# Optimization experiments

Hardware: AMD Instinct MI355X
Metric: run time of the kernel (lower is better)

## Reference

```python
import jax, jax.numpy as jnp
import numpy as np

B, L = 128, 100
VOCAB, WORD_D = 50000, 100
TAG_NUM, TAG_D = 52, 20
POS_NUM, POS_D = 202, 20
HID = 256                 # hidden_size = NUM_CAPS * CAP_D
NUM_CAPS, CAP_D = 16, 16
N_CLASS = 19
ROUTING_ITER = 3
IN_D = WORD_D + TAG_D + 2 * POS_D  # 160
ENTITY_MARK = 68          # pos value marking the entity token


def setup_inputs() -> dict:
    key = jax.random.key(0)
    ks = jax.random.split(key, 20)
    s = 0.05
    word = jax.random.randint(ks[0], (B, L), 0, VOCAB)
    tag = jax.random.randint(ks[1], (B, L), 0, TAG_NUM)
    pos1 = jax.random.randint(ks[2], (B, L), 0, POS_NUM)
    pos2 = jax.random.randint(ks[3], (B, L), 0, POS_NUM)
    # guarantee exactly one ENTITY_MARK per row (getEntityFeature's .index(68))
    pos1 = jnp.where(pos1 == ENTITY_MARK, ENTITY_MARK + 1, pos1)
    pos2 = jnp.where(pos2 == ENTITY_MARK, ENTITY_MARK + 1, pos2)
    e1 = jax.random.randint(ks[4], (B,), 0, L)
    e2 = jax.random.randint(ks[5], (B,), 0, L)
    pos1 = pos1.at[jnp.arange(B), e1].set(ENTITY_MARK)
    pos2 = pos2.at[jnp.arange(B), e2].set(ENTITY_MARK)
    # embedding tables (padding_idx 0 rows zeroed for tag/pos, as in torch)
    word_emb = jax.random.normal(ks[6], (VOCAB, WORD_D), jnp.float32) * s
    tag_emb = (jax.random.normal(ks[7], (TAG_NUM, TAG_D), jnp.float32) * s).at[0].set(0.0)
    pos1_emb = (jax.random.normal(ks[8], (POS_NUM, POS_D), jnp.float32) * s).at[0].set(0.0)
    pos2_emb = (jax.random.normal(ks[9], (POS_NUM, POS_D), jnp.float32) * s).at[0].set(0.0)
    # BiLSTM params (torch gate order i,f,g,o stacked along first axis)
    def lstm_params(k):
        k1, k2 = jax.random.split(k)
        w_ih = jax.random.normal(k1, (4 * HID, IN_D), jnp.float32) * s
        w_hh = jax.random.normal(k2, (4 * HID, HID), jnp.float32) * s
        return w_ih, w_hh, jnp.zeros((4 * HID,), jnp.float32), jnp.zeros((4 * HID,), jnp.float32)
    w_ih_f, w_hh_f, b_ih_f, b_hh_f = lstm_params(ks[10])
    w_ih_b, w_hh_b, b_ih_b, b_hh_b = lstm_params(ks[11])
    # digit-caps transform [in_caps, in_dim, out_caps*out_dim]
    W_caps = jax.random.normal(ks[12], (NUM_CAPS * L, CAP_D, N_CLASS * CAP_D), jnp.float32) * s
    b_route = jnp.zeros((NUM_CAPS * L, N_CLASS), jnp.float32)  # routing logit prior (learned)
    return {"word": word, "tag": tag, "pos1": pos1, "pos2": pos2,
            "word_emb": word_emb, "tag_emb": tag_emb, "pos1_emb": pos1_emb, "pos2_emb": pos2_emb,
            "w_ih_f": w_ih_f, "w_hh_f": w_hh_f, "b_ih_f": b_ih_f, "b_hh_f": b_hh_f,
            "w_ih_b": w_ih_b, "w_hh_b": w_hh_b, "b_ih_b": b_ih_b, "b_hh_b": b_hh_b,
            "W_caps": W_caps, "b_route": b_route}


def _lstm_dir(x, w_ih, w_hh, b_ih, b_hh, reverse):
    # x: [B, L, IN_D] -> h: [B, L, HID]
    xg = jnp.einsum('bld,gd->blg', x, w_ih) + b_ih + b_hh  # precompute input gates
    def step(carry, g):
        h, c = carry
        g = g + h @ w_hh.T
        i, f, gg, o = jnp.split(g, 4, axis=-1)
        c = jax.nn.sigmoid(f) * c + jax.nn.sigmoid(i) * jnp.tanh(gg)
        h = jax.nn.sigmoid(o) * jnp.tanh(c)
        return (h, c), h
    init = (jnp.zeros((x.shape[0], HID), x.dtype), jnp.zeros((x.shape[0], HID), x.dtype))
    _, hs = jax.lax.scan(step, init, jnp.swapaxes(xg, 0, 1), reverse=reverse)
    return jnp.swapaxes(hs, 0, 1)


def _squash(x, axis=-1):
    n2 = jnp.sum(x * x, axis=axis, keepdims=True)
    return x * (n2 / (1.0 + n2)) / jnp.sqrt(n2 + 1e-9)


def reference(word, tag, pos1, pos2, word_emb, tag_emb, pos1_emb, pos2_emb,
              w_ih_f, w_hh_f, b_ih_f, b_hh_f, w_ih_b, w_hh_b, b_ih_b, b_hh_b,
              W_caps, b_route):
    # embed + concat (dropout = identity in eval mode)
    emb = jnp.concatenate([word_emb[word], tag_emb[tag], pos1_emb[pos1], pos2_emb[pos2]], axis=-1)
    hf = _lstm_dir(emb, w_ih_f, w_hh_f, b_ih_f, b_hh_f, reverse=False)
    hb = _lstm_dir(emb, w_ih_b, w_hh_b, b_ih_b, b_hh_b, reverse=True)
    x = hf + hb  # sum of direction halves == x[:,:,:H] + x[:,:,H:2H]
    # vectorized entity gather: first index where pos == 68
    bidx = jnp.arange(x.shape[0])
    e1 = jnp.argmax(pos1 == ENTITY_MARK, axis=1)
    e2 = jnp.argmax(pos2 == ENTITY_MARK, axis=1)
    he = x[bidx, e1] + x[bidx, e2]  # [B, HID]
    # primary capsules: [B, L*NUM_CAPS, CAP_D], squashed per capsule
    u = _squash(x.reshape(x.shape[0], L * NUM_CAPS, CAP_D))
    # entity-guided attention over words, broadcast to capsules
    att = jax.nn.softmax(jnp.einsum('bld,bd->bl', x, he), axis=1)  # [B, L]
    alpha = jnp.repeat(att, NUM_CAPS, axis=1)  # [B, L*NUM_CAPS]
    # digit caps predictions: [B, in_caps, N_CLASS, CAP_D]
    u_hat = jnp.einsum('bic,ico->bio', u, W_caps).reshape(x.shape[0], L * NUM_CAPS, N_CLASS, CAP_D)
    # attention-weighted agreement routing
    bb = jnp.broadcast_to(b_route, (x.shape[0],) + b_route.shape)
    v = None
    for _ in range(ROUTING_ITER):
        c = jax.nn.softmax(bb, axis=-1) * alpha[:, :, None]  # coupling * attention
        s = jnp.einsum('bio,biod->bod', c, u_hat)
        v = _squash(s)  # [B, N_CLASS, CAP_D]
        bb = bb + jnp.einsum('biod,bod->bio', u_hat, v)
    # class probabilities = capsule lengths
    return jnp.sqrt(jnp.sum(v * v, axis=2) + 1e-9)
```

## Files before the change

### kernel.cpp

```cpp
#include <hip/hip_runtime.h>
#include <math.h>

#define B_     128
#define L_     100
#define HID_   256
#define IND_   160
#define NCLASS 19
#define CAPD   16
#define NI     1600
#define OD     304
#define ENTITY 68

#define SLDS   24

typedef _Float16 half2_t __attribute__((ext_vector_type(2)));

__device__ inline half2_t as_h2(unsigned u) {
    union { unsigned u; half2_t h; } x; x.u = u; return x.h;
}
__device__ inline unsigned pack2(float a, float b) {
    union { unsigned u; half2_t h; } x;
    x.h = (half2_t){ (_Float16)a, (_Float16)b };
    return x.u;
}
__device__ inline float fdot2_(unsigned w, unsigned h, float acc) {
#if __has_builtin(__builtin_amdgcn_fdot2)
    return __builtin_amdgcn_fdot2(as_h2(w), as_h2(h), acc, false);
#else
    half2_t wh = as_h2(w), hh = as_h2(h);
    acc = fmaf((float)wh.x, (float)hh.x, acc);
    return fmaf((float)wh.y, (float)hh.y, acc);
#endif
}

__global__ void emb_gather(const int* __restrict__ word, const int* __restrict__ tag,
                           const int* __restrict__ pos1, const int* __restrict__ pos2,
                           const float* __restrict__ we, const float* __restrict__ te,
                           const float* __restrict__ p1e, const float* __restrict__ p2e,
                           float* __restrict__ emb)
{
    int idx = blockIdx.x * 256 + threadIdx.x;
    int bt = idx / IND_;
    int k  = idx - bt * IND_;
    float v;
    if (k < 100)      v = we[word[bt] * 100 + k];
    else if (k < 120) v = te[tag[bt] * 20 + (k - 100)];
    else if (k < 140) v = p1e[pos1[bt] * 20 + (k - 120)];
    else              v = p2e[pos2[bt] * 20 + (k - 140)];
    emb[idx] = v;
}

__global__ void __launch_bounds__(256) gemm_xg(
    const float* __restrict__ emb,
    const float* __restrict__ wihf, const float* __restrict__ bihf, const float* __restrict__ bhhf,
    const float* __restrict__ wihb, const float* __restrict__ bihb, const float* __restrict__ bhhb,
    float* __restrict__ xg)
{
    int gt  = blockIdx.x;
    int t   = blockIdx.y;
    int dir = blockIdx.z;
    const float* w  = dir ? wihb : wihf;
    const float* bi = dir ? bihb : bihf;
    const float* bh = dir ? bhhb : bhhf;
    int gj0 = gt * 128;

    __shared__ float wsh[32][132];
    __shared__ float esh[32][132];

    int tid = threadIdx.x;
    int tx = tid & 15, ty = tid >> 4;

    float acc[8][8];
    #pragma unroll
    for (int i = 0; i < 8; ++i)
        #pragma unroll
        for (int j = 0; j < 8; ++j) acc[i][j] = 0.f;

    for (int k0 = 0; k0 < IND_; k0 += 32) {
        __syncthreads();
        #pragma unroll
        for (int m = 0; m < 16; ++m) {
            int e = m * 256 + tid;
            int k = e & 31, g = e >> 5;
            wsh[k][g] = w[(gj0 + g) * IND_ + k0 + k];
            esh[k][g] = emb[(g * L_ + t) * IND_ + k0 + k];
        }
        __syncthreads();
        #pragma unroll
        for (int k = 0; k < 32; ++k) {
            float wv[8], ev[8];
            #pragma unroll
            for (int q = 0; q < 8; ++q) wv[q] = wsh[k][ty * 8 + q];
            #pragma unroll
            for (int q = 0; q < 8; ++q) ev[q] = esh[k][tx * 8 + q];
            #pragma unroll
            for (int i = 0; i < 8; ++i)
                #pragma unroll
                for (int j = 0; j < 8; ++j) acc[i][j] = fmaf(wv[i], ev[j], acc[i][j]);
        }
    }
    #pragma unroll
    for (int i = 0; i < 8; ++i) {
        int gj = gj0 + ty * 8 + i;
        float bias = bi[gj] + bh[gj];
        #pragma unroll
        for (int j = 0; j < 8; ++j) {
            int b = tx * 8 + j;
            xg[((((size_t)dir * L_ + t) * 64 + (b >> 1)) * 1024 + gj) * 2 + (b & 1)]
                = acc[i][j] + bias;
        }
    }
}

__global__ void whh_pack16(const float* __restrict__ whhf, const float* __restrict__ whhb,
                           unsigned* __restrict__ wp)
{
    int gid = blockIdx.x * 256 + threadIdx.x;
    int g   = gid & 3;
    int h   = (gid >> 2) & 255;
    int p   = (gid >> 10) & 127;
    int dir = gid >> 17;
    const float* whh = dir ? whhb : whhf;
    const float* row = whh + (size_t)(g * 256 + h) * HID_;
    wp[gid] = pack2(row[2 * p], row[2 * p + 1]);
}

__global__ void __launch_bounds__(1024, 4) lstm_scan_s(
    const float* __restrict__ xg, const uint4* __restrict__ wp16,
    float* __restrict__ xf2, float* __restrict__ xb2)
{
    int blk = blockIdx.x;
    int dir = blk >> 6;
    int bp  = blk & 63;
    int tid = threadIdx.x;
    int h   = tid & 255;
    int q   = tid >> 8;

    const uint4* wt = wp16 + (size_t)dir * 128 * 256;
    float* xo = dir ? xb2 : xf2;

    __shared__ uint2 hA[128];
    __shared__ uint2 hB[128];
    __shared__ float pbuf[4][8][256];
    __shared__ uint4 wlds[SLDS][256];

    for (int m = q; m < SLDS; m += 4)
        wlds[m][h] = wt[m * 256 + h];

    if (tid < 256) ((unsigned*)hA)[tid] = 0u;
    float c0 = 0.f, c1 = 0.f;
    __syncthreads();

    int pq0  = q * 32;
    int sbeg = (q == 0) ? SLDS : pq0;
    int send = pq0 + 32;

    for (int t = 0; t < L_; ++t) {
        int slot = dir ? (L_ - 1 - t) : t;
        const uint2* hp = (t & 1) ? hB : hA;
        unsigned*    hw = (unsigned*)((t & 1) ? hA : hB);

        float2 gI, gF, gG, gO;
        if (q == 0) {
            const float* xbase = xg + (((size_t)dir * L_ + slot) * 64 + bp) * 2048;
            gI = *(const float2*)(xbase + (0 * 256 + h) * 2);
            gF = *(const float2*)(xbase + (1 * 256 + h) * 2);
            gG = *(const float2*)(xbase + (2 * 256 + h) * 2);
            gO = *(const float2*)(xbase + (3 * 256 + h) * 2);
        }

        float aI0=0.f, aI1=0.f, aF0=0.f, aF1=0.f;
        float aG0=0.f, aG1=0.f, aO0=0.f, aO1=0.f;

        #pragma unroll 8
        for (int p = sbeg; p < send; ++p) {
            uint4 w4 = wt[p * 256 + h];
            uint2 hb = hp[p];
            aI0 = fdot2_(w4.x, hb.x, aI0); aI1 = fdot2_(w4.x, hb.y, aI1);
            aF0 = fdot2_(w4.y, hb.x, aF0); aF1 = fdot2_(w4.y, hb.y, aF1);
            aG0 = fdot2_(w4.z, hb.x, aG0); aG1 = fdot2_(w4.z, hb.y, aG1);
            aO0 = fdot2_(w4.w, hb.x, aO0); aO1 = fdot2_(w4.w, hb.y, aO1);
        }
        if (q == 0) {
            #pragma unroll 8
            for (int p = 0; p < SLDS; ++p) {
                uint4 w4 = wlds[p][h];
                uint2 hb = hp[p];
                aI0 = fdot2_(w4.x, hb.x, aI0); aI1 = fdot2_(w4.x, hb.y, aI1);
                aF0 = fdot2_(w4.y, hb.x, aF0); aF1 = fdot2_(w4.y, hb.y, aF1);
                aG0 = fdot2_(w4.z, hb.x, aG0); aG1 = fdot2_(w4.z, hb.y, aG1);
                aO0 = fdot2_(w4.w, hb.x, aO0); aO1 = fdot2_(w4.w, hb.y, aO1);
            }
        }

        pbuf[q][0][h] = aI0; pbuf[q][1][h] = aI1;
        pbuf[q][2][h] = aF0; pbuf[q][3][h] = aF1;
        pbuf[q][4][h] = aG0; pbuf[q][5][h] = aG1;
        pbuf[q][6][h] = aO0; pbuf[q][7][h] = aO1;
        __syncthreads();

        if (q == 0) {
            float sI0 = pbuf[0][0][h] + pbuf[1][0][h] + pbuf[2][0][h] + pbuf[3][0][h] + gI.x;
            float sI1 = pbuf[0][1][h] + pbuf[1][1][h] + pbuf[2][1][h] + pbuf[3][1][h] + gI.y;
            float sF0 = pbuf[0][2][h] + pbuf[1][2][h] + pbuf[2][2][h] + pbuf[3][2][h] + gF.x;
            float sF1 = pbuf[0][3][h] + pbuf[1][3][h] + pbuf[2][3][h] + pbuf[3][3][h] + gF.y;
            float sG0 = pbuf[0][4][h] + pbuf[1][4][h] + pbuf[2][4][h] + pbuf[3][4][h] + gG.x;
            float sG1 = pbuf[0][5][h] + pbuf[1][5][h] + pbuf[2][5][h] + pbuf[3][5][h] + gG.y;
            float sO0 = pbuf[0][6][h] + pbuf[1][6][h] + pbuf[2][6][h] + pbuf[3][6][h] + gO.x;
            float sO1 = pbuf[0][7][h] + pbuf[1][7][h] + pbuf[2][7][h] + pbuf[3][7][h] + gO.y;

            float i0 = 1.f / (1.f + expf(-sI0));
            float f0 = 1.f / (1.f + expf(-sF0));
            float g0 = tanhf(sG0);
            float o0 = 1.f / (1.f + expf(-sO0));
            c0 = f0 * c0 + i0 * g0;
            float hv0 = o0 * tanhf(c0);

            float i1 = 1.f / (1.f + expf(-sI1));
            float f1 = 1.f / (1.f + expf(-sF1));
            float g1 = tanhf(sG1);
            float o1 = 1.f / (1.f + expf(-sO1));
            c1 = f1 * c1 + i1 * g1;
            float hv1 = o1 * tanhf(c1);

            float n0 = __shfl_xor(hv0, 1);
            float n1 = __shfl_xor(hv1, 1);
            hw[h] = (h & 1) ? pack2(n1, hv1)
                            : pack2(hv0, n0);
            float* xp = xo + ((size_t)slot * 64 + bp) * 512 + h * 2;
            xp[0] = hv0; xp[1] = hv1;
        }
        __syncthreads();
    }
}

__global__ void x_add(const float* __restrict__ xf2, const float* __restrict__ xb2,
                      float* __restrict__ x)
{
    int idx = blockIdx.x * 256 + threadIdx.x;
    int b    = idx & 127;
    int j    = (idx >> 7) & 255;
    int slot = idx >> 15;
    int src  = ((slot * 64 + (b >> 1)) * 512) + j * 2 + (b & 1);
    x[idx] = xf2[src] + xb2[src];
}

__global__ void wc_pack16(const float* __restrict__ W, unsigned* __restrict__ wc)
{
    int gid = blockIdx.x * 256 + threadIdx.x;
    int od  = gid % OD;
    int rest = gid / OD;
    int cp  = rest & 7;
    int i   = rest >> 3;
    float a = W[((size_t)i * 16 + 2 * cp) * OD + od];
    float b = W[((size_t)i * 16 + 2 * cp + 1) * OD + od];
    wc[gid] = pack2(a, b);
}

__global__ void find_entity(const int* __restrict__ pos1, const int* __restrict__ pos2,
                            int* __restrict__ e)
{
    int b = threadIdx.x;
    int e1 = 0, e2 = 0;
    for (int l = L_ - 1; l >= 0; --l) if (pos1[b * L_ + l] == ENTITY) e1 = l;
    for (int l = L_ - 1; l >= 0; --l) if (pos2[b * L_ + l] == ENTITY) e2 = l;
    e[b] = e1; e[B_ + b] = e2;
}

__global__ void compute_he(const float* __restrict__ x, const int* __restrict__ e,
                           float* __restrict__ he)
{
    int j = blockIdx.x, b = threadIdx.x;
    int e1 = e[b], e2 = e[B_ + b];
    he[j * B_ + b] = x[((size_t)e1 * HID_ + j) * B_ + b] + x[((size_t)e2 * HID_ + j) * B_ + b];
}

__global__ void att_logits(const float* __restrict__ x, const float* __restrict__ he,
                           float* __restrict__ logits)
{
    int l = blockIdx.x, b = threadIdx.x;
    float acc = 0.f;
    for (int j = 0; j < HID_; ++j)
        acc = fmaf(x[((size_t)l * HID_ + j) * B_ + b], he[j * B_ + b], acc);
    logits[l * B_ + b] = acc;
}

__global__ void att_softmax(const float* __restrict__ logits, float* __restrict__ att)
{
    int b = threadIdx.x;
    float m = -1e30f;
    for (int l = 0; l < L_; ++l) m = fmaxf(m, logits[l * B_ + b]);
    float s = 0.f;
    for (int l = 0; l < L_; ++l) s += expf(logits[l * B_ + b] - m);
    float inv = 1.f / s;
    for (int l = 0; l < L_; ++l) att[l * B_ + b] = expf(logits[l * B_ + b] - m) * inv;
}

__global__ void u_squash16(const float* __restrict__ x, unsigned* __restrict__ u16)
{
    int i = blockIdx.x, b = threadIdx.x;
    int l = i >> 4, cap = i & 15;
    float vals[16]; float n2 = 0.f;
    #pragma unroll
    for (int c2 = 0; c2 < 16; ++c2) {
        float v = x[((size_t)l * HID_ + cap * 16 + c2) * B_ + b];
        vals[c2] = v; n2 = fmaf(v, v, n2);
    }
    float f = (n2 / (1.f + n2)) / sqrtf(n2 + 1e-9f);
    #pragma unroll
    for (int cp = 0; cp < 8; ++cp)
        u16[((size_t)i * B_ + b) * 8 + cp] = pack2(vals[2 * cp] * f, vals[2 * cp + 1] * f);
}

__global__ void bb_init(const float* __restrict__ br, float* __restrict__ bb)
{
    int idx = blockIdx.x * 256 + threadIdx.x;
    bb[idx] = br[idx % (NI * NCLASS)];
}

__global__ void __launch_bounds__(320) s_pass16(
    const unsigned* __restrict__ u16, const unsigned* __restrict__ Wc16,
    const float* __restrict__ bb, const float* __restrict__ att,
    float* __restrict__ partial)
{
    int ic = blockIdx.x, bt = blockIdx.y;
    int i0 = ic * 16, b0 = bt * 16;
    __shared__ float C[16][16][20];
    int tid = threadIdx.x;
    if (tid < 256) {
        int bl = tid >> 4, il = tid & 15;
        int b = b0 + bl, i = i0 + il;
        const float* bbp = bb + ((size_t)b * NI + i) * NCLASS;
        float m = bbp[0];
        #pragma unroll
        for (int o = 1; o < NCLASS; ++o) m = fmaxf(m, bbp[o]);
        float s = 0.f; float e[NCLASS];
        #pragma unroll
        for (int o = 0; o < NCLASS; ++o) { e[o] = expf(bbp[o] - m); s += e[o]; }
        float al = att[(i >> 4) * B_ + b] / s;
        #pragma unroll
        for (int o = 0; o < NCLASS; ++o) C[bl][il][o] = e[o] * al;
    }
    __syncthreads();
    if (tid >= OD) return;
    int od = tid, o = od >> 4;
    float acc[16];
    #pragma unroll
    for (int bl = 0; bl < 16; ++bl) acc[bl] = 0.f;
    for (int il = 0; il < 16; ++il) {
        int i = i0 + il;
        const unsigned* wp = Wc16 + (size_t)i * 8 * OD + od;
        unsigned w2[8];
        #pragma unroll
        for (int cp = 0; cp < 8; ++cp) w2[cp] = wp[cp * OD];
        const unsigned* up = u16 + ((size_t)i * B_ + b0) * 8;
        #pragma unroll
        for (int bl = 0; bl < 16; ++bl) {
            float uh = 0.f;
            #pragma unroll
            for (int cp = 0; cp < 8; ++cp) uh = fdot2_(up[bl * 8 + cp], w2[cp], uh);
            acc[bl] = fmaf(C[bl][il][o], uh, acc[bl]);
        }
    }
    #pragma unroll
    for (int bl = 0; bl < 16; ++bl)
        partial[((size_t)ic * B_ + b0 + bl) * OD + od] = acc[bl];
}

__global__ void s_reduce(const float* __restrict__ partial, float* __restrict__ s)
{
    int idx = blockIdx.x * 256 + threadIdx.x;
    int b = idx / OD, od = idx - b * OD;
    float acc = 0.f;
    for (int ic = 0; ic < 100; ++ic) acc += partial[((size_t)ic * B_ + b) * OD + od];
    s[idx] = acc;
}

__global__ void squash_v(const float* __restrict__ s, float* __restrict__ v,
                         float* __restrict__ out, int write_out)
{
    int idx = blockIdx.x * 256 + threadIdx.x;
    if (idx >= B_ * NCLASS) return;
    const float* sp = s + (size_t)idx * 16;
    float vals[16]; float n2 = 0.f;
    #pragma unroll
    for (int d = 0; d < 16; ++d) { vals[d] = sp[d]; n2 = fmaf(vals[d], vals[d], n2); }
    float f = (n2 / (1.f + n2)) / sqrtf(n2 + 1e-9f);
    float n2v = 0.f;
    #pragma unroll
    for (int d = 0; d < 16; ++d) {
        float vv = vals[d] * f;
        v[(size_t)idx * 16 + d] = vv;
        n2v = fmaf(vv, vv, n2v);
    }
    if (write_out) out[idx] = sqrtf(n2v + 1e-9f);
}

__global__ void __launch_bounds__(320) bb_pass16(
    const unsigned* __restrict__ u16, const unsigned* __restrict__ Wc16,
    const float* __restrict__ v, float* __restrict__ bb)
{
    int ic = blockIdx.x, bt = blockIdx.y;
    int i0 = ic * 16, b0 = bt * 16;
    int tid = threadIdx.x;
    if (tid >= OD) return;
    int od = tid, o = od >> 4, d = od & 15;
    float vv[16];
    #pragma unroll
    for (int bl = 0; bl < 16; ++bl) vv[bl] = v[(size_t)(b0 + bl) * OD + od];
    for (int il = 0; il < 16; ++il) {
        int i = i0 + il;
        const unsigned* wp = Wc16 + (size_t)i * 8 * OD + od;
        unsigned w2[8];
        #pragma unroll
        for (int cp = 0; cp < 8; ++cp) w2[cp] = wp[cp * OD];
        const unsigned* up = u16 + ((size_t)i * B_ + b0) * 8;
        #pragma unroll
        for (int bl = 0; bl < 16; ++bl) {
            float uh = 0.f;
            #pragma unroll
            for (int cp = 0; cp < 8; ++cp) uh = fdot2_(up[bl * 8 + cp], w2[cp], uh);
            float p = uh * vv[bl];
            p += __shfl_xor(p, 1);
            p += __shfl_xor(p, 2);
            p += __shfl_xor(p, 4);
            p += __shfl_xor(p, 8);
            if (d == 0) bb[((size_t)(b0 + bl) * NI + i) * NCLASS + o] += p;
        }
    }
}

extern "C" void kernel_launch(void* const* d_in, const int* in_sizes, int n_in,
                              void* d_out, int out_size, void* d_ws, size_t ws_size,
                              hipStream_t stream)
{
    (void)in_sizes; (void)n_in; (void)out_size; (void)ws_size;
    const int*   word = (const int*)d_in[0];
    const int*   tag  = (const int*)d_in[1];
    const int*   pos1 = (const int*)d_in[2];
    const int*   pos2 = (const int*)d_in[3];
    const float* we   = (const float*)d_in[4];
    const float* te   = (const float*)d_in[5];
    const float* p1e  = (const float*)d_in[6];
    const float* p2e  = (const float*)d_in[7];
    const float* wihf = (const float*)d_in[8];
    const float* whhf = (const float*)d_in[9];
    const float* bihf = (const float*)d_in[10];
    const float* bhhf = (const float*)d_in[11];
    const float* wihb = (const float*)d_in[12];
    const float* whhb = (const float*)d_in[13];
    const float* bihb = (const float*)d_in[14];
    const float* bhhb = (const float*)d_in[15];
    const float* Wc   = (const float*)d_in[16];
    const float* br   = (const float*)d_in[17];

    float* wsp    = (float*)d_ws;
    float* emb    = wsp;
    float* xg     = wsp + 2048000;
    float* xf     = xg + 26214400;
    float* xb     = xf + 3276800;
    float* he     = xb + 3276800;
    float* logits = he + 32768;
    float* att    = logits + 12800;
    int*   e      = (int*)(att + 12800);
    unsigned* wp16 = (unsigned*)emb;
    unsigned* Wc16 = (unsigned*)xf;
    float*    x    = xg;
    unsigned* u16  = (unsigned*)(xg + 3276800);
    float*    bb   = xg + 6553600;
    float*    part = xg + 10444800;
    float*    s    = xg + 14336000;
    float*    v    = s + 38912;
    float*    out  = (float*)d_out;

    emb_gather<<<8000, 256, 0, stream>>>(word, tag, pos1, pos2, we, te, p1e, p2e, emb);
    gemm_xg<<<dim3(8, 100, 2), 256, 0, stream>>>(emb, wihf, bihf, bhhf, wihb, bihb, bhhb, xg);
    whh_pack16<<<1024, 256, 0, stream>>>(whhf, whhb, wp16);
    lstm_scan_s<<<128, 1024, 0, stream>>>(xg, (const uint4*)wp16, xf, xb);
    x_add<<<12800, 256, 0, stream>>>(xf, xb, x);
    wc_pack16<<<15200, 256, 0, stream>>>(Wc, Wc16);
    find_entity<<<1, 128, 0, stream>>>(pos1, pos2, e);
    compute_he<<<256, 128, 0, stream>>>(x, e, he);
    att_logits<<<100, 128, 0, stream>>>(x, he, logits);
    att_softmax<<<1, 128, 0, stream>>>(logits, att);
    u_squash16<<<1600, 128, 0, stream>>>(x, u16);
    bb_init<<<15200, 256, 0, stream>>>(br, bb);
    for (int it = 0; it < 3; ++it) {
        s_pass16<<<dim3(100, 8), 320, 0, stream>>>(u16, Wc16, bb, att, part);
        s_reduce<<<152, 256, 0, stream>>>(part, s);
        squash_v<<<10, 256, 0, stream>>>(s, v, out, (it == 2) ? 1 : 0);
        if (it < 2) bb_pass16<<<dim3(100, 8), 320, 0, stream>>>(u16, Wc16, v, bb);
    }
}
```

Measured before the change: 1.174 ms.

## Use fp16 dot2 input GEMM, fold bb init, parallelize attention softmax

```diff
diff --git a/kernel.cpp b/kernel.cpp
--- a/kernel.cpp
+++ b/kernel.cpp
@@ -33,39 +33,53 @@
 #endif
 }
 
-__global__ void emb_gather(const int* __restrict__ word, const int* __restrict__ tag,
-                           const int* __restrict__ pos1, const int* __restrict__ pos2,
-                           const float* __restrict__ we, const float* __restrict__ te,
-                           const float* __restrict__ p1e, const float* __restrict__ p2e,
-                           float* __restrict__ emb)
+__global__ void emb_gather16(const int* __restrict__ word, const int* __restrict__ tag,
+                             const int* __restrict__ pos1, const int* __restrict__ pos2,
+                             const float* __restrict__ we, const float* __restrict__ te,
+                             const float* __restrict__ p1e, const float* __restrict__ p2e,
+                             unsigned* __restrict__ emb16)
 {
     int idx = blockIdx.x * 256 + threadIdx.x;
-    int bt = idx / IND_;
-    int k  = idx - bt * IND_;
-    float v;
-    if (k < 100)      v = we[word[bt] * 100 + k];
-    else if (k < 120) v = te[tag[bt] * 20 + (k - 100)];
-    else if (k < 140) v = p1e[pos1[bt] * 20 + (k - 120)];
-    else              v = p2e[pos2[bt] * 20 + (k - 140)];
-    emb[idx] = v;
-}
-
-__global__ void __launch_bounds__(256) gemm_xg(
-    const float* __restrict__ emb,
-    const float* __restrict__ wihf, const float* __restrict__ bihf, const float* __restrict__ bhhf,
-    const float* __restrict__ wihb, const float* __restrict__ bihb, const float* __restrict__ bhhb,
+    int bt = idx / 80;
+    int kp = idx - bt * 80;
+    int k  = 2 * kp;
+    float v0, v1;
+    if (k < 100)      { const float* p = we  + word[bt] * 100 + k;         v0 = p[0]; v1 = p[1]; }
+    else if (k < 120) { const float* p = te  + tag[bt]  * 20 + (k - 100);  v0 = p[0]; v1 = p[1]; }
+    else if (k < 140) { const float* p = p1e + pos1[bt] * 20 + (k - 120);  v0 = p[0]; v1 = p[1]; }
+    else              { const float* p = p2e + pos2[bt] * 20 + (k - 140);  v0 = p[0]; v1 = p[1]; }
+    emb16[idx] = pack2(v0, v1);
+}
+
+__global__ void wih_pack16(const float* __restrict__ wihf, const float* __restrict__ wihb,
+                           unsigned* __restrict__ wp)
+{
+    int gid = blockIdx.x * 256 + threadIdx.x;
+    int dir = gid / 81920;
+    int rem = gid - dir * 81920;
+    int kp  = rem >> 10;
+    int gj  = rem & 1023;
+    const float* w = dir ? wihb : wihf;
+    const float* row = w + (size_t)gj * IND_ + 2 * kp;
+    wp[gid] = pack2(row[0], row[1]);
+}
+
+__global__ void __launch_bounds__(256) gemm_xg16(
+    const unsigned* __restrict__ emb16, const unsigned* __restrict__ wih16,
+    const float* __restrict__ bihf, const float* __restrict__ bhhf,
+    const float* __restrict__ bihb, const float* __restrict__ bhhb,
     float* __restrict__ xg)
 {
     int gt  = blockIdx.x;
     int t   = blockIdx.y;
     int dir = blockIdx.z;
-    const float* w  = dir ? wihb : wihf;
+    const unsigned* wbase = wih16 + (size_t)dir * 81920;
     const float* bi = dir ? bihb : bihf;
     const float* bh = dir ? bhhb : bhhf;
     int gj0 = gt * 128;
 
-    __shared__ float wsh[32][132];
-    __shared__ float esh[32][132];
+    __shared__ unsigned wsh[16][132];
+    __shared__ unsigned esh[16][132];
 
     int tid = threadIdx.x;
     int tx = tid & 15, ty = tid >> 4;
@@ -76,27 +90,28 @@
         #pragma unroll
         for (int j = 0; j < 8; ++j) acc[i][j] = 0.f;
 
-    for (int k0 = 0; k0 < IND_; k0 += 32) {
+    for (int kp0 = 0; kp0 < 80; kp0 += 16) {
         __syncthreads();
         #pragma unroll
-        for (int m = 0; m < 16; ++m) {
+        for (int m = 0; m < 8; ++m) {
             int e = m * 256 + tid;
-            int k = e & 31, g = e >> 5;
-            wsh[k][g] = w[(gj0 + g) * IND_ + k0 + k];
-            esh[k][g] = emb[(g * L_ + t) * IND_ + k0 + k];
+            int kw = e >> 7, gw = e & 127;
+            wsh[kw][gw] = wbase[(kp0 + kw) * 1024 + gj0 + gw];
+            int ke = e & 15, ge = e >> 4;
+            esh[ke][ge] = emb16[((size_t)ge * L_ + t) * 80 + kp0 + ke];
         }
         __syncthreads();
         #pragma unroll
-        for (int k = 0; k < 32; ++k) {
-            float wv[8], ev[8];
+        for (int kp = 0; kp < 16; ++kp) {
+            unsigned wv[8], ev[8];
             #pragma unroll
-            for (int q = 0; q < 8; ++q) wv[q] = wsh[k][ty * 8 + q];
+            for (int q = 0; q < 8; ++q) wv[q] = wsh[kp][ty * 8 + q];
             #pragma unroll
-            for (int q = 0; q < 8; ++q) ev[q] = esh[k][tx * 8 + q];
+            for (int q = 0; q < 8; ++q) ev[q] = esh[kp][tx * 8 + q];
             #pragma unroll
             for (int i = 0; i < 8; ++i)
                 #pragma unroll
-                for (int j = 0; j < 8; ++j) acc[i][j] = fmaf(wv[i], ev[j], acc[i][j]);
+                for (int j = 0; j < 8; ++j) acc[i][j] = fdot2_(wv[i], ev[j], acc[i][j]);
         }
     }
     #pragma unroll
@@ -257,43 +272,56 @@
     wc[gid] = pack2(a, b);
 }
 
-__global__ void find_entity(const int* __restrict__ pos1, const int* __restrict__ pos2,
-                            int* __restrict__ e)
-{
-    int b = threadIdx.x;
+__global__ void compute_he2(const int* __restrict__ pos1, const int* __restrict__ pos2,
+                            const float* __restrict__ x, float* __restrict__ he)
+{
+    int j = blockIdx.x, b = threadIdx.x;
     int e1 = 0, e2 = 0;
     for (int l = L_ - 1; l >= 0; --l) if (pos1[b * L_ + l] == ENTITY) e1 = l;
     for (int l = L_ - 1; l >= 0; --l) if (pos2[b * L_ + l] == ENTITY) e2 = l;
-    e[b] = e1; e[B_ + b] = e2;
-}
-
-__global__ void compute_he(const float* __restrict__ x, const int* __restrict__ e,
-                           float* __restrict__ he)
-{
-    int j = blockIdx.x, b = threadIdx.x;
-    int e1 = e[b], e2 = e[B_ + b];
     he[j * B_ + b] = x[((size_t)e1 * HID_ + j) * B_ + b] + x[((size_t)e2 * HID_ + j) * B_ + b];
 }
 
-__global__ void att_logits(const float* __restrict__ x, const float* __restrict__ he,
-                           float* __restrict__ logits)
-{
-    int l = blockIdx.x, b = threadIdx.x;
+__global__ void att_logits2(const float* __restrict__ x, const float* __restrict__ he,
+                            float* __restrict__ lp)
+{
+    int l = blockIdx.x, jc = blockIdx.y, b = threadIdx.x;
+    int j0 = jc * 32;
     float acc = 0.f;
-    for (int j = 0; j < HID_; ++j)
+    #pragma unroll
+    for (int jj = 0; jj < 32; ++jj) {
+        int j = j0 + jj;
         acc = fmaf(x[((size_t)l * HID_ + j) * B_ + b], he[j * B_ + b], acc);
-    logits[l * B_ + b] = acc;
-}
-
-__global__ void att_softmax(const float* __restrict__ logits, float* __restrict__ att)
-{
-    int b = threadIdx.x;
-    float m = -1e30f;
-    for (int l = 0; l < L_; ++l) m = fmaxf(m, logits[l * B_ + b]);
-    float s = 0.f;
-    for (int l = 0; l < L_; ++l) s += expf(logits[l * B_ + b] - m);
-    float inv = 1.f / s;
-    for (int l = 0; l < L_; ++l) att[l * B_ + b] = expf(logits[l * B_ + b] - m) * inv;
+    }
+    lp[((size_t)jc * L_ + l) * B_ + b] = acc;
+}
+
+__global__ void att_softmax2(const float* __restrict__ lp, float* __restrict__ att)
+{
+    int b = blockIdx.x, l = threadIdx.x;
+    float val = 0.f;
+    if (l < L_) {
+        #pragma unroll
+        for (int jc = 0; jc < 8; ++jc) val += lp[((size_t)jc * L_ + l) * B_ + b];
+    }
+    __shared__ float red[128];
+    red[l] = (l < L_) ? val : -1e30f;
+    __syncthreads();
+    for (int off = 64; off > 0; off >>= 1) {
+        if (l < off) red[l] = fmaxf(red[l], red[l + off]);
+        __syncthreads();
+    }
+    float m = red[0];
+    __syncthreads();
+    float e = (l < L_) ? expf(val - m) : 0.f;
+    red[l] = e;
+    __syncthreads();
+    for (int off = 64; off > 0; off >>= 1) {
+        if (l < off) red[l] += red[l + off];
+        __syncthreads();
+    }
+    float inv = 1.f / red[0];
+    if (l < L_) att[l * B_ + b] = e * inv;
 }
 
 __global__ void u_squash16(const float* __restrict__ x, unsigned* __restrict__ u16)
@@ -312,16 +340,10 @@
         u16[((size_t)i * B_ + b) * 8 + cp] = pack2(vals[2 * cp] * f, vals[2 * cp + 1] * f);
 }
 
-__global__ void bb_init(const float* __restrict__ br, float* __restrict__ bb)
-{
-    int idx = blockIdx.x * 256 + threadIdx.x;
-    bb[idx] = br[idx % (NI * NCLASS)];
-}
-
 __global__ void __launch_bounds__(320) s_pass16(
     const unsigned* __restrict__ u16, const unsigned* __restrict__ Wc16,
-    const float* __restrict__ bb, const float* __restrict__ att,
-    float* __restrict__ partial)
+    const float* __restrict__ bb, const float* __restrict__ br, int first,
+    const float* __restrict__ att, float* __restrict__ partial)
 {
     int ic = blockIdx.x, bt = blockIdx.y;
     int i0 = ic * 16, b0 = bt * 16;
@@ -330,7 +352,8 @@
     if (tid < 256) {
         int bl = tid >> 4, il = tid & 15;
         int b = b0 + bl, i = i0 + il;
-        const float* bbp = bb + ((size_t)b * NI + i) * NCLASS;
+        const float* bbp = first ? (br + (size_t)i * NCLASS)
+                                 : (bb + ((size_t)b * NI + i) * NCLASS);
         float m = bbp[0];
         #pragma unroll
         for (int o = 1; o < NCLASS; ++o) m = fmaxf(m, bbp[o]);
@@ -398,7 +421,8 @@
 
 __global__ void __launch_bounds__(320) bb_pass16(
     const unsigned* __restrict__ u16, const unsigned* __restrict__ Wc16,
-    const float* __restrict__ v, float* __restrict__ bb)
+    const float* __restrict__ v, float* __restrict__ bb,
+    const float* __restrict__ br, int first)
 {
     int ic = blockIdx.x, bt = blockIdx.y;
     int i0 = ic * 16, b0 = bt * 16;
@@ -425,7 +449,10 @@
             p += __shfl_xor(p, 2);
             p += __shfl_xor(p, 4);
             p += __shfl_xor(p, 8);
-            if (d == 0) bb[((size_t)(b0 + bl) * NI + i) * NCLASS + o] += p;
+            if (d == 0) {
+                size_t off = ((size_t)(b0 + bl) * NI + i) * NCLASS + o;
+                bb[off] = (first ? br[(size_t)i * NCLASS + o] : bb[off]) + p;
+            }
         }
     }
 }
@@ -454,17 +481,17 @@
     const float* Wc   = (const float*)d_in[16];
     const float* br   = (const float*)d_in[17];
 
-    float* wsp    = (float*)d_ws;
-    float* emb    = wsp;
-    float* xg     = wsp + 2048000;
-    float* xf     = xg + 26214400;
-    float* xb     = xf + 3276800;
-    float* he     = xb + 3276800;
-    float* logits = he + 32768;
-    float* att    = logits + 12800;
-    int*   e      = (int*)(att + 12800);
-    unsigned* wp16 = (unsigned*)emb;
+    float* wsp = (float*)d_ws;
+    unsigned* emb16 = (unsigned*)wsp;
+    unsigned* wih16 = (unsigned*)(wsp + 1024000);
+    unsigned* wp16  = (unsigned*)(wsp + 1024000 + 163840);
+    float* xg  = wsp + 2048000;
+    float* xf  = xg + 26214400;
+    float* xb  = xf + 3276800;
+    float* he  = xb + 3276800;
+    float* att = he + 32768;
     unsigned* Wc16 = (unsigned*)xf;
+    float*    lp   = xf + 3891200;
     float*    x    = xg;
     unsigned* u16  = (unsigned*)(xg + 3276800);
     float*    bb   = xg + 6553600;
@@ -473,22 +500,21 @@
     float*    v    = s + 38912;
     float*    out  = (float*)d_out;
 
-    emb_gather<<<8000, 256, 0, stream>>>(word, tag, pos1, pos2, we, te, p1e, p2e, emb);
-    gemm_xg<<<dim3(8, 100, 2), 256, 0, stream>>>(emb, wihf, bihf, bhhf, wihb, bihb, bhhb, xg);
+    emb_gather16<<<4000, 256, 0, stream>>>(word, tag, pos1, pos2, we, te, p1e, p2e, emb16);
+    wih_pack16<<<640, 256, 0, stream>>>(wihf, wihb, wih16);
     whh_pack16<<<1024, 256, 0, stream>>>(whhf, whhb, wp16);
+    gemm_xg16<<<dim3(8, 100, 2), 256, 0, stream>>>(emb16, wih16, bihf, bhhf, bihb, bhhb, xg);
     lstm_scan_s<<<128, 1024, 0, stream>>>(xg, (const uint4*)wp16, xf, xb);
     x_add<<<12800, 256, 0, stream>>>(xf, xb, x);
     wc_pack16<<<15200, 256, 0, stream>>>(Wc, Wc16);
-    find_entity<<<1, 128, 0, stream>>>(pos1, pos2, e);
-    compute_he<<<256, 128, 0, stream>>>(x, e, he);
-    att_logits<<<100, 128, 0, stream>>>(x, he, logits);
-    att_softmax<<<1, 128, 0, stream>>>(logits, att);
+    compute_he2<<<256, 128, 0, stream>>>(pos1, pos2, x, he);
+    att_logits2<<<dim3(100, 8), 128, 0, stream>>>(x, he, lp);
+    att_softmax2<<<128, 128, 0, stream>>>(lp, att);
     u_squash16<<<1600, 128, 0, stream>>>(x, u16);
-    bb_init<<<15200, 256, 0, stream>>>(br, bb);
     for (int it = 0; it < 3; ++it) {
-        s_pass16<<<dim3(100, 8), 320, 0, stream>>>(u16, Wc16, bb, att, part);
+        s_pass16<<<dim3(100, 8), 320, 0, stream>>>(u16, Wc16, bb, br, it == 0, att, part);
         s_reduce<<<152, 256, 0, stream>>>(part, s);
         squash_v<<<10, 256, 0, stream>>>(s, v, out, (it == 2) ? 1 : 0);
-        if (it < 2) bb_pass16<<<dim3(100, 8), 320, 0, stream>>>(u16, Wc16, v, bb);
-    }
-}
+        if (it < 2) bb_pass16<<<dim3(100, 8), 320, 0, stream>>>(u16, Wc16, v, bb, br, it == 0);
+    }
+}
```

New measurement: 1.089 ms. -7.3%, faster.
